# Performance work log

Hardware: AMD Instinct MI355X
Metric: run time of the kernel (lower is better)

The kernel has to match this reference:

```python
import jax, jax.numpy as jnp
import numpy as np

# Dims per init_kwargs
B, C_IN, H, W = 64, 512, 28, 28
GROWTH, BN_SIZE = 32, 4
C_MID = BN_SIZE * GROWTH  # 128
EPS = 1e-5
NUM_BITS = 8          # activation & weight quantization bits
NUM_CHUNKS = 16       # RangeBN chunking (eladhoffer quantize.py default)


def quantize(x, num_bits):
    """Uniform min/max quantize-dequantize (UniformQuantize forward)."""
    mn = x.min()
    mx = x.max()
    qmax = 2.0 ** num_bits - 1.0
    scale = jnp.maximum((mx - mn) / qmax, 1e-8)
    q = jnp.round((jnp.clip(x, mn, mx) - mn) / scale)
    return q * scale + mn


def conv2d(x, w, pad):
    return jax.lax.conv_general_dilated(
        x, w, window_strides=(1, 1), padding=[(pad, pad), (pad, pad)],
        dimension_numbers=('NCHW', 'OIHW', 'NCHW'))


def batchnorm2d(x, w, b):
    # training-mode BN: batch statistics over (N,H,W), biased variance
    mean = x.mean(axis=(0, 2, 3), keepdims=True)
    var = x.var(axis=(0, 2, 3), keepdims=True)
    xhat = (x - mean) * jax.lax.rsqrt(var + EPS)
    return xhat * w.reshape(1, -1, 1, 1) + b.reshape(1, -1, 1, 1)


def range_bn(x, w, b):
    # Range-based BN (training-mode): per-channel mean, scale from chunked min/max range
    Bx, Cx, Hx, Wx = x.shape
    y = x.transpose(1, 0, 2, 3).reshape(Cx, NUM_CHUNKS, -1)  # [C, chunks, n]
    mean_max = y.max(-1).mean(-1)   # [C]
    mean_min = y.min(-1).mean(-1)   # [C]
    mean = y.reshape(Cx, -1).mean(-1)  # [C]
    n = y.shape[-1]
    scale_fix = (0.5 * 0.35) * (1.0 + (np.pi * np.log(4.0)) ** 0.5) / ((2.0 * np.log(float(n))) ** 0.5)
    scale = 1.0 / ((mean_max - mean_min) * scale_fix + EPS)
    out = (x - mean.reshape(1, Cx, 1, 1)) * scale.reshape(1, Cx, 1, 1)
    qw = quantize(w, NUM_BITS)
    qb = quantize(b, NUM_BITS)
    return out * qw.reshape(1, Cx, 1, 1) + qb.reshape(1, Cx, 1, 1)


def setup_inputs() -> dict:
    key = jax.random.key(0)
    ks = jax.random.split(key, 7)
    x = jax.random.normal(ks[0], (B, C_IN, H, W), dtype=jnp.float32)
    bn1_w = jax.random.uniform(ks[1], (C_IN,), dtype=jnp.float32, minval=0.5, maxval=1.5)
    bn1_b = jax.random.normal(ks[2], (C_IN,), dtype=jnp.float32) * 0.1
    conv1_w = jax.random.normal(ks[3], (C_MID, C_IN, 1, 1), dtype=jnp.float32) * (2.0 / C_IN) ** 0.5
    rbn_w = jax.random.uniform(ks[4], (C_MID,), dtype=jnp.float32, minval=0.5, maxval=1.5)
    rbn_b = jax.random.normal(ks[5], (C_MID,), dtype=jnp.float32) * 0.1
    conv2_w = jax.random.normal(ks[6], (GROWTH, C_MID, 3, 3), dtype=jnp.float32) * (2.0 / (9 * C_MID)) ** 0.5
    return {"x": x, "bn1_w": bn1_w, "bn1_b": bn1_b, "conv1_w": conv1_w,
            "rbn_w": rbn_w, "rbn_b": rbn_b, "conv2_w": conv2_w}


def reference(x, bn1_w, bn1_b, conv1_w, rbn_w, rbn_b, conv2_w):
    # norm1 -> relu1 -> QConv2d(1x1) -> RangeBN -> relu2 -> QConv2d(3x3) -> concat
    h = jax.nn.relu(batchnorm2d(x, bn1_w, bn1_b))
    h = conv2d(quantize(h, NUM_BITS), quantize(conv1_w, NUM_BITS), pad=0)
    h = jax.nn.relu(range_bn(h, rbn_w, rbn_b))
    h = conv2d(quantize(h, NUM_BITS), quantize(conv2_w, NUM_BITS), pad=1)
    # drop_rate = 0 -> dropout is identity
    return jnp.concatenate([x, h], axis=1)
```

## Files before the change

kernel.cpp:

```cpp
#include <hip/hip_runtime.h>
#include <math.h>

static constexpr int BB    = 64;
static constexpr int C_IN  = 512;
static constexpr int C_MID = 128;
static constexpr int C_OUT = 32;
static constexpr int C_TOT = 544;
static constexpr int HW    = 784;

static constexpr size_t H2_OFF    = 0;
static constexpr size_t QW1_OFF   = 6422528;
static constexpr size_t QW2_OFF   = QW1_OFF + 65536;
static constexpr size_t PSTAT_OFF = QW2_OFF + 49152;
static constexpr size_t BNA_OFF   = PSTAT_OFF + 16384;
static constexpr size_t BNB_OFF   = BNA_OFF + 512;
static constexpr size_t A2_OFF    = BNB_OFF + 512;
static constexpr size_t B2_OFF    = A2_OFF + 128;
static constexpr size_t QRW_OFF   = B2_OFF + 128;
static constexpr size_t QRB_OFF   = QRW_OFF + 128;
static constexpr size_t SCAL_OFF  = QRB_OFF + 128;
static constexpr size_t PART_OFF  = SCAL_OFF + 16;
static constexpr size_t RP_OFF    = PART_OFF + 128;
static constexpr size_t PART2_OFF = RP_OFF + 172032;

#define DEVFN __device__ __forceinline__

typedef __bf16 bf16x8 __attribute__((ext_vector_type(8)));
typedef float  f32x4  __attribute__((ext_vector_type(4)));

DEVFN float qact(float v, float mn, float mx, float inv, float sc) {
    v = fminf(fmaxf(v, mn), mx);
    return fmaf(rintf((v - mn) * inv), sc, mn);
}

DEVFN unsigned f2bf(float f) {
    unsigned u = __float_as_uint(f);
    return (u + 0x7fffu + ((u >> 16) & 1u)) >> 16;
}

DEVFN float bf2f(unsigned short h) { return __uint_as_float((unsigned)h << 16); }

__global__ __launch_bounds__(256) void k_stats(const float* __restrict__ x,
                                               const float* __restrict__ conv1_w,
                                               const float* __restrict__ conv2_w,
                                               float* __restrict__ ws) {
    const int bid = blockIdx.x, tid = threadIdx.x;
    __shared__ float r0[256], r1[256], r2[256], r3[256];

    if (bid < 4096) {
        const int xcd = bid & 7, slot = bid >> 3;
        const int c = xcd * 64 + (slot & 63), bg = slot >> 6;
        float s = 0.f, s2 = 0.f, mn = INFINITY, mx = -INFINITY;
        for (int i = tid; i < 1568; i += 256) {
            const int b = bg * 8 + i / 196, j = i % 196;
            const float4 v = ((const float4*)(x + ((size_t)b * C_IN + c) * HW))[j];
            s  += (v.x + v.y) + (v.z + v.w);
            s2 += v.x * v.x + v.y * v.y + v.z * v.z + v.w * v.w;
            mn = fminf(mn, fminf(fminf(v.x, v.y), fminf(v.z, v.w)));
            mx = fmaxf(mx, fmaxf(fmaxf(v.x, v.y), fmaxf(v.z, v.w)));
        }
        r0[tid] = s; r1[tid] = s2; r2[tid] = mn; r3[tid] = mx;
        __syncthreads();
        for (int off = 128; off > 0; off >>= 1) {
            if (tid < off) {
                r0[tid] += r0[tid + off];
                r1[tid] += r1[tid + off];
                r2[tid] = fminf(r2[tid], r2[tid + off]);
                r3[tid] = fmaxf(r3[tid], r3[tid + off]);
            }
            __syncthreads();
        }
        if (tid == 0) {
            float* p = ws + PSTAT_OFF + ((size_t)c * 8 + bg) * 4;
            p[0] = r0[0]; p[1] = r1[0]; p[2] = r2[0]; p[3] = r3[0];
        }
    } else {
        const int wb = bid - 4096;
        float mn = INFINITY, mx = -INFINITY;
        if (wb < 32) {
            const float4* src = (const float4*)conv1_w + (size_t)wb * 512;
            for (int i = tid; i < 512; i += 256) {
                const float4 v = src[i];
                mn = fminf(mn, fminf(fminf(v.x, v.y), fminf(v.z, v.w)));
                mx = fmaxf(mx, fmaxf(fmaxf(v.x, v.y), fmaxf(v.z, v.w)));
            }
        } else {
            const float4* src = (const float4*)conv2_w + (size_t)(wb - 32) * 1152;
            for (int i = tid; i < 1152; i += 256) {
                const float4 v = src[i];
                mn = fminf(mn, fminf(fminf(v.x, v.y), fminf(v.z, v.w)));
                mx = fmaxf(mx, fmaxf(fmaxf(v.x, v.y), fmaxf(v.z, v.w)));
            }
        }
        r2[tid] = mn; r3[tid] = mx;
        __syncthreads();
        for (int off = 128; off > 0; off >>= 1) {
            if (tid < off) { r2[tid] = fminf(r2[tid], r2[tid + off]); r3[tid] = fmaxf(r3[tid], r3[tid + off]); }
            __syncthreads();
        }
        if (tid == 0) {
            float* p = (wb < 32) ? ws + PART_OFF + (size_t)wb * 2
                                 : ws + PART_OFF + 64 + (size_t)(wb - 32) * 2;
            p[0] = r2[0]; p[1] = r3[0];
        }
    }
}

__global__ __launch_bounds__(256) void k_prep(const float* __restrict__ conv1_w,
                                              const float* __restrict__ conv2_w,
                                              const float* __restrict__ bn1_w,
                                              const float* __restrict__ bn1_b,
                                              const float* __restrict__ rbn_w,
                                              const float* __restrict__ rbn_b,
                                              float* __restrict__ ws) {
    const int b = blockIdx.x, tid = threadIdx.x;
    __shared__ float ra[256], rb[256];
    __shared__ float s_mn, s_sc;

    if (b < 32) {
        ra[tid] = tid < 32 ? ws[PART_OFF + tid * 2] : INFINITY;
        rb[tid] = tid < 32 ? ws[PART_OFF + tid * 2 + 1] : -INFINITY;
        __syncthreads();
        for (int off = 128; off > 0; off >>= 1) {
            if (tid < off) { ra[tid] = fminf(ra[tid], ra[tid + off]); rb[tid] = fmaxf(rb[tid], rb[tid + off]); }
            __syncthreads();
        }
        if (tid == 0) { s_mn = ra[0]; s_sc = fmaxf((rb[0] - ra[0]) / 255.f, 1e-8f); }
        __syncthreads();
        const float mnw = s_mn, scw = s_sc;
        unsigned short* qw = (unsigned short*)(ws + QW1_OFF);
        const int base = b * 2048;
#pragma unroll
        for (int t = 0; t < 8; ++t) {
            const int i = base + t * 256 + tid;
            const int co = i >> 9, k = i & 511;
            const float v = conv1_w[i];
            const float qv = fmaf(rintf((v - mnw) / scw), scw, mnw);
            const int ks = k >> 6, kc = (k >> 3) & 7, klo = k & 7;
            qw[(((size_t)ks * 128 + co) << 6) + (((kc ^ (co & 7)) << 3) | klo)] = (unsigned short)f2bf(qv);
        }
    } else if (b < 40) {
        ra[tid] = tid < 8 ? ws[PART_OFF + 64 + tid * 2] : INFINITY;
        rb[tid] = tid < 8 ? ws[PART_OFF + 64 + tid * 2 + 1] : -INFINITY;
        __syncthreads();
        for (int off = 128; off > 0; off >>= 1) {
            if (tid < off) { ra[tid] = fminf(ra[tid], ra[tid + off]); rb[tid] = fmaxf(rb[tid], rb[tid + off]); }
            __syncthreads();
        }
        if (tid == 0) { s_mn = ra[0]; s_sc = fmaxf((rb[0] - ra[0]) / 255.f, 1e-8f); }
        __syncthreads();
        const float mnw = s_mn, scw = s_sc;
        unsigned short* qw2 = (unsigned short*)(ws + QW2_OFF);
        const int base = (b - 32) * 4608;
        for (int i2 = tid; i2 < 4608; i2 += 256) {
            const int i = base + i2;
            const int co = i / 1152, r = i % 1152, ci = r / 9, tap = r % 9;
            const float v = conv2_w[i];
            const float qv = fmaf(rintf((v - mnw) / scw), scw, mnw);
            qw2[(size_t)co * 1152 + tap * 128 + ci] = (unsigned short)f2bf(qv);
        }
    } else if (b == 40) {
        float lmn = INFINITY, lmx = -INFINITY;
        for (int c = tid; c < 512; c += 256) {
            const float* p = ws + PSTAT_OFF + (size_t)c * 32;
            float s = 0.f, s2 = 0.f, cmn = INFINITY, cmx = -INFINITY;
            for (int g = 0; g < 8; ++g) {
                s += p[g * 4 + 0]; s2 += p[g * 4 + 1];
                cmn = fminf(cmn, p[g * 4 + 2]); cmx = fmaxf(cmx, p[g * 4 + 3]);
            }
            const float n = 50176.f;
            const float mean = s / n;
            const float var  = s2 / n - mean * mean;
            const float rstd = rsqrtf(var + 1e-5f);
            const float A  = rstd * bn1_w[c];
            const float Bc = bn1_b[c] - mean * A;
            ws[BNA_OFF + c] = A; ws[BNB_OFF + c] = Bc;
            const float v1 = A * cmn + Bc, v2 = A * cmx + Bc;
            lmn = fminf(lmn, fmaxf(0.f, fminf(v1, v2)));
            lmx = fmaxf(lmx, fmaxf(0.f, fmaxf(v1, v2)));
        }
        ra[tid] = lmn; rb[tid] = lmx;
        __syncthreads();
        for (int off = 128; off > 0; off >>= 1) {
            if (tid < off) { ra[tid] = fminf(ra[tid], ra[tid + off]); rb[tid] = fmaxf(rb[tid], rb[tid + off]); }
            __syncthreads();
        }
        if (tid == 0) {
            const float mn1 = ra[0], mx1 = rb[0];
            const float sc = fmaxf((mx1 - mn1) / 255.f, 1e-8f);
            ws[SCAL_OFF + 0] = mn1; ws[SCAL_OFF + 1] = sc; ws[SCAL_OFF + 2] = 1.f / sc; ws[SCAL_OFF + 6] = mx1;
        }
    } else {
        for (int which = 0; which < 2; ++which) {
            const float* src = which ? rbn_b : rbn_w;
            const size_t dst = which ? QRB_OFF : QRW_OFF;
            float v = 0.f;
            ra[tid] = INFINITY; rb[tid] = -INFINITY;
            if (tid < 128) { v = src[tid]; ra[tid] = v; rb[tid] = v; }
            __syncthreads();
            for (int off = 128; off > 0; off >>= 1) {
                if (tid < off) { ra[tid] = fminf(ra[tid], ra[tid + off]); rb[tid] = fmaxf(rb[tid], rb[tid + off]); }
                __syncthreads();
            }
            if (tid == 0) { s_mn = ra[0]; s_sc = fmaxf((rb[0] - ra[0]) / 255.f, 1e-8f); }
            __syncthreads();
            if (tid < 128) ws[dst + tid] = fmaf(rintf((v - s_mn) / s_sc), s_sc, s_mn);
            __syncthreads();
        }
    }
}

__global__ __launch_bounds__(256, 2) void k_conv1(const float* __restrict__ x,
                                                  float* __restrict__ out,
                                                  float* __restrict__ ws) {
    __shared__ __align__(16) unsigned short wt[128 * 64];
    __shared__ __align__(16) unsigned short ht[112 * 64];
    const int tid = threadIdx.x;
    const int pt = blockIdx.x, b = blockIdx.y;
    const int p0 = pt * 112;
    const float mn1 = ws[SCAL_OFF + 0], sc1 = ws[SCAL_OFF + 1];
    const float inv1 = ws[SCAL_OFF + 2];
    const unsigned short* qw1 = (const unsigned short*)(ws + QW1_OFF);
    const float* xb = x + (size_t)b * C_IN * HW;
    float* outb = out + (size_t)b * C_TOT * HW;

    const int o = tid & 7, q = tid >> 3;
    const int wv = tid >> 6, g = (tid >> 4) & 3, r4 = tid & 15;

    f32x4 acc[2][7];
#pragma unroll
    for (int i = 0; i < 2; ++i)
#pragma unroll
        for (int j = 0; j < 7; ++j) acc[i][j] = f32x4{0.f, 0.f, 0.f, 0.f};

    f32x4 xreg[8];
    if (tid < 224) {
#pragma unroll
        for (int j = 0; j < 8; ++j)
            xreg[j] = *(const f32x4*)(xb + (size_t)(o * 8 + j) * HW + p0 + q * 4);
    }

    for (int ks = 0; ks < 8; ++ks) {
        const float4* wsrc = (const float4*)(qw1 + (size_t)ks * 8192);
        float4* wdst = (float4*)wt;
#pragma unroll
        for (int i = 0; i < 4; ++i) wdst[tid + i * 256] = wsrc[tid + i * 256];

        if (tid < 224) {
            const int ci0 = ks * 64 + o * 8;
            float vv[8][4];
#pragma unroll
            for (int j = 0; j < 8; ++j) {
                const f32x4 v = xreg[j];
                __builtin_nontemporal_store(v, (f32x4*)(outb + (size_t)(ci0 + j) * HW + p0 + q * 4));
                const float A = ws[BNA_OFF + ci0 + j], Bc = ws[BNB_OFF + ci0 + j];
                vv[j][0] = fmaf(rintf((fmaxf(fmaf(v.x, A, Bc), 0.f) - mn1) * inv1), sc1, mn1);
                vv[j][1] = fmaf(rintf((fmaxf(fmaf(v.y, A, Bc), 0.f) - mn1) * inv1), sc1, mn1);
                vv[j][2] = fmaf(rintf((fmaxf(fmaf(v.z, A, Bc), 0.f) - mn1) * inv1), sc1, mn1);
                vv[j][3] = fmaf(rintf((fmaxf(fmaf(v.w, A, Bc), 0.f) - mn1) * inv1), sc1, mn1);
            }
            if (ks < 7) {
                const int ci0n = (ks + 1) * 64 + o * 8;
#pragma unroll
                for (int j = 0; j < 8; ++j)
                    xreg[j] = *(const f32x4*)(xb + (size_t)(ci0n + j) * HW + p0 + q * 4);
            }
#pragma unroll
            for (int r = 0; r < 4; ++r) {
                const int p = q * 4 + r;
                uint4 pk;
                pk.x = f2bf(vv[0][r]) | (f2bf(vv[1][r]) << 16);
                pk.y = f2bf(vv[2][r]) | (f2bf(vv[3][r]) << 16);
                pk.z = f2bf(vv[4][r]) | (f2bf(vv[5][r]) << 16);
                pk.w = f2bf(vv[6][r]) | (f2bf(vv[7][r]) << 16);
                *(uint4*)&ht[p * 64 + ((o ^ (p & 7)) << 3)] = pk;
            }
        }
        __syncthreads();

#pragma unroll
        for (int ksub = 0; ksub < 2; ++ksub) {
            const int kk = ksub * 4 + g;
            bf16x8 af[2], bfr[7];
#pragma unroll
            for (int ct = 0; ct < 2; ++ct) {
                const int co = wv * 32 + ct * 16 + r4;
                af[ct] = *(const bf16x8*)&wt[co * 64 + ((kk ^ (co & 7)) << 3)];
            }
#pragma unroll
            for (int pf = 0; pf < 7; ++pf) {
                const int p = pf * 16 + r4;
                bfr[pf] = *(const bf16x8*)&ht[p * 64 + ((kk ^ (p & 7)) << 3)];
            }
#pragma unroll
            for (int ct = 0; ct < 2; ++ct)
#pragma unroll
                for (int pf = 0; pf < 7; ++pf)
                    acc[ct][pf] = __builtin_amdgcn_mfma_f32_16x16x32_bf16(af[ct], bfr[pf], acc[ct][pf], 0, 0, 0);
        }
        __syncthreads();
    }

    unsigned short* hb = (unsigned short*)(ws + H2_OFF) + (size_t)b * C_MID * HW;
#pragma unroll
    for (int ct = 0; ct < 2; ++ct) {
        const int co0 = wv * 32 + ct * 16 + g * 4;
#pragma unroll
        for (int pf = 0; pf < 7; ++pf) {
            const int p = p0 + pf * 16 + r4;
#pragma unroll
            for (int r = 0; r < 4; ++r)
                hb[(size_t)(co0 + r) * HW + p] = (unsigned short)f2bf(acc[ct][pf][r]);
        }
    }

#pragma unroll
    for (int ct = 0; ct < 2; ++ct)
#pragma unroll
        for (int r = 0; r < 4; ++r) {
            float s = 0.f, mn = INFINITY, mx = -INFINITY;
#pragma unroll
            for (int pf = 0; pf < 7; ++pf) {
                const float v = acc[ct][pf][r];
                s += v; mn = fminf(mn, v); mx = fmaxf(mx, v);
            }
#pragma unroll
            for (int m = 1; m < 16; m <<= 1) {
                s  += __shfl_xor(s, m, 64);
                mn  = fminf(mn, __shfl_xor(mn, m, 64));
                mx  = fmaxf(mx, __shfl_xor(mx, m, 64));
            }
            if (r4 == 0) {
                const int co = wv * 32 + ct * 16 + g * 4 + r;
                float* dst = ws + RP_OFF + (((size_t)co * 64 + b) * 7 + pt) * 3;
                dst[0] = s; dst[1] = mn; dst[2] = mx;
            }
        }
}

__global__ __launch_bounds__(64) void k_rbn_combine(float* __restrict__ ws) {
    const int c = blockIdx.x, t = threadIdx.x;
    const int ch = t >> 2, sub = t & 3;
    const int b = ch * 4 + sub;
    const float* rp = ws + RP_OFF + ((size_t)c * 64 + b) * 21;
    float s = 0.f, mn = INFINITY, mx = -INFINITY;
#pragma unroll
    for (int pt = 0; pt < 7; ++pt) {
        s += rp[pt * 3 + 0];
        mn = fminf(mn, rp[pt * 3 + 1]);
        mx = fmaxf(mx, rp[pt * 3 + 2]);
    }
#pragma unroll
    for (int m = 1; m < 4; m <<= 1) {
        s  += __shfl_xor(s, m, 64);
        mn  = fminf(mn, __shfl_xor(mn, m, 64));
        mx  = fmaxf(mx, __shfl_xor(mx, m, 64));
    }
    float smx = mx, smn = mn, stot = s, gmn = mn, gmx = mx;
#pragma unroll
    for (int m = 4; m < 64; m <<= 1) {
        smx  += __shfl_xor(smx, m, 64);
        smn  += __shfl_xor(smn, m, 64);
        stot += __shfl_xor(stot, m, 64);
        gmn   = fminf(gmn, __shfl_xor(gmn, m, 64));
        gmx   = fmaxf(gmx, __shfl_xor(gmx, m, 64));
    }
    if (t == 0) {
        const float mm = smx * (1.f / 16.f), mnm = smn * (1.f / 16.f);
        const float mean = stot / 50176.f;
        const double PI_D = 3.14159265358979323846;
        const double sfd = 0.175 * (1.0 + sqrt(PI_D * log(4.0))) / sqrt(2.0 * log(3136.0));
        const float scale = 1.f / ((mm - mnm) * (float)sfd + 1e-5f);
        const float A  = scale * ws[QRW_OFF + c];
        const float Bc = ws[QRB_OFF + c] - mean * A;
        ws[A2_OFF + c] = A; ws[B2_OFF + c] = Bc;
        const float v1 = A * gmn + Bc, v2 = A * gmx + Bc;
        ws[PART2_OFF + c * 2 + 0] = fmaxf(0.f, fminf(v1, v2));
        ws[PART2_OFF + c * 2 + 1] = fmaxf(0.f, fmaxf(v1, v2));
    }
}

__global__ __launch_bounds__(256, 2) void k_conv2(float* __restrict__ out, const float* __restrict__ ws) {
    __shared__ __align__(16) unsigned short lact[7 * 30 * 128];
    __shared__ float sra[128], srb[128];
    __shared__ float s_mn3, s_mx3, s_sc3, s_inv3;
    const int tid = threadIdx.x;
    const int pt = blockIdx.x, b = blockIdx.y;
    const int y0 = pt * 4;

    if (tid < 128) { sra[tid] = ws[PART2_OFF + tid * 2]; srb[tid] = ws[PART2_OFF + tid * 2 + 1]; }
    __syncthreads();
    for (int off = 64; off > 0; off >>= 1) {
        if (tid < off) { sra[tid] = fminf(sra[tid], sra[tid + off]); srb[tid] = fmaxf(srb[tid], srb[tid + off]); }
        __syncthreads();
    }
    if (tid == 0) {
        const float mn3 = sra[0], mx3 = srb[0];
        const float sc = fmaxf((mx3 - mn3) / 255.f, 1e-8f);
        s_mn3 = mn3; s_mx3 = mx3; s_sc3 = sc; s_inv3 = 1.f / sc;
    }
    {
        const uint4 z = {0u, 0u, 0u, 0u};
        uint4* lp = (uint4*)lact;
        for (int i = tid; i < 3360; i += 256) lp[i] = z;
    }
    __syncthreads();
    const float mn3 = s_mn3, mx3 = s_mx3, sc3 = s_sc3, inv3 = s_inv3;

    const unsigned short* h2b = (const unsigned short*)(ws + H2_OFF) + (size_t)b * C_MID * HW;
    for (int task = tid; task < 672; task += 256) {
        const int oct = task / 42, rem = task % 42, r = rem / 7, xq = rem % 7;
        const int gy = y0 - 1 + r;
        if (gy < 0 || gy > 27) continue;
        float vv[8][4];
#pragma unroll
        for (int j = 0; j < 8; ++j) {
            const int ci = oct * 8 + j;
            const ushort4 v = *(const ushort4*)(h2b + (size_t)ci * HW + gy * 28 + xq * 4);
            const float A = ws[A2_OFF + ci], Bc = ws[B2_OFF + ci];
            vv[j][0] = qact(fmaxf(0.f, fmaf(bf2f(v.x), A, Bc)), mn3, mx3, inv3, sc3);
            vv[j][1] = qact(fmaxf(0.f, fmaf(bf2f(v.y), A, Bc)), mn3, mx3, inv3, sc3);
            vv[j][2] = qact(fmaxf(0.f, fmaf(bf2f(v.z), A, Bc)), mn3, mx3, inv3, sc3);
            vv[j][3] = qact(fmaxf(0.f, fmaf(bf2f(v.w), A, Bc)), mn3, mx3, inv3, sc3);
        }
#pragma unroll
        for (int xi = 0; xi < 4; ++xi) {
            const int col = xq * 4 + xi + 1;
            const int phys = (oct + col) & 15;
            uint4 pk;
            pk.x = f2bf(vv[0][xi]) | (f2bf(vv[1][xi]) << 16);
            pk.y = f2bf(vv[2][xi]) | (f2bf(vv[3][xi]) << 16);
            pk.z = f2bf(vv[4][xi]) | (f2bf(vv[5][xi]) << 16);
            pk.w = f2bf(vv[6][xi]) | (f2bf(vv[7][xi]) << 16);
            *(uint4*)&lact[((r * 30 + col) * 16 + phys) * 8] = pk;
        }
    }
    __syncthreads();

    const int wv = tid >> 6, lane = tid & 63, r4 = lane & 15, g = lane >> 4;
    int py[2], px[2];
#pragma unroll
    for (int i = 0; i < 2; ++i) {
        const int p = (wv * 2 + i) * 16 + r4;
        py[i] = p / 28; px[i] = p % 28;
    }
    f32x4 acc[2][2];
#pragma unroll
    for (int ct = 0; ct < 2; ++ct)
#pragma unroll
        for (int i = 0; i < 2; ++i) acc[ct][i] = f32x4{0.f, 0.f, 0.f, 0.f};

    const unsigned short* qw2 = (const unsigned short*)(ws + QW2_OFF);
    for (int tap = 0; tap < 9; ++tap) {
        const int dy = tap / 3, dx = tap % 3;
        bf16x8 afr[2][4];
#pragma unroll
        for (int ct = 0; ct < 2; ++ct)
#pragma unroll
            for (int c4 = 0; c4 < 4; ++c4) {
                const int co = ct * 16 + r4;
                afr[ct][c4] = *(const bf16x8*)&qw2[(size_t)co * 1152 + tap * 128 + c4 * 32 + g * 8];
            }
#pragma unroll
        for (int c4 = 0; c4 < 4; ++c4) {
            bf16x8 bfr[2];
#pragma unroll
            for (int i = 0; i < 2; ++i) {
                const int row = py[i] + dy, col = px[i] + dx;
                const int phys = (c4 * 4 + g + col) & 15;
                bfr[i] = *(const bf16x8*)&lact[((row * 30 + col) * 16 + phys) * 8];
            }
#pragma unroll
            for (int ct = 0; ct < 2; ++ct)
#pragma unroll
                for (int i = 0; i < 2; ++i)
                    acc[ct][i] = __builtin_amdgcn_mfma_f32_16x16x32_bf16(afr[ct][c4], bfr[i], acc[ct][i], 0, 0, 0);
        }
    }

#pragma unroll
    for (int ct = 0; ct < 2; ++ct)
#pragma unroll
        for (int i = 0; i < 2; ++i) {
            const int pf = wv * 2 + i;
            if (pf < 7) {
                const int p = pf * 16 + r4;
#pragma unroll
                for (int r = 0; r < 4; ++r) {
                    const int co = ct * 16 + g * 4 + r;
                    out[((size_t)b * C_TOT + 512 + co) * HW + y0 * 28 + p] = acc[ct][i][r];
                }
            }
        }
}

extern "C" void kernel_launch(void* const* d_in, const int* in_sizes, int n_in,
                              void* d_out, int out_size, void* d_ws, size_t ws_size,
                              hipStream_t stream) {
    const float* x       = (const float*)d_in[0];
    const float* bn1_w   = (const float*)d_in[1];
    const float* bn1_b   = (const float*)d_in[2];
    const float* conv1_w = (const float*)d_in[3];
    const float* rbn_w   = (const float*)d_in[4];
    const float* rbn_b   = (const float*)d_in[5];
    const float* conv2_w = (const float*)d_in[6];
    float* out = (float*)d_out;
    float* ws  = (float*)d_ws;

    k_stats<<<4136, 256, 0, stream>>>(x, conv1_w, conv2_w, ws);
    k_prep<<<42, 256, 0, stream>>>(conv1_w, conv2_w, bn1_w, bn1_b, rbn_w, rbn_b, ws);
    k_conv1<<<dim3(7, 64), 256, 0, stream>>>(x, out, ws);
    k_rbn_combine<<<128, 64, 0, stream>>>(ws);
    k_conv2<<<dim3(7, 64), 256, 0, stream>>>(out, ws);
}
```

Before: 103.2 us.

## Store intermediate activations channel-last via LDS transpose for coalesced conv2 staging

The conv1 epilogue now transposes its bf16 accumulator tile through shared memory so the intermediate tensor is written in pixel-major (NHWC) layout with 16-byte coalesced stores, replacing scattered 2-byte channel-major writes. The conv2 staging loop reads 8 contiguous channels per pixel with one 16-byte load and takes per-channel affine coefficients from shared memory instead of repeated global loads. This targets uncoalesced global traffic in both kernels, at the cost of an extra LDS round trip and barrier in conv1.

```diff
diff --git a/kernel.cpp b/kernel.cpp
--- a/kernel.cpp
+++ b/kernel.cpp
@@ -213,8 +213,9 @@
 __global__ __launch_bounds__(256, 2) void k_conv1(const float* __restrict__ x,
                                                   float* __restrict__ out,
                                                   float* __restrict__ ws) {
-    __shared__ __align__(16) unsigned short wt[128 * 64];
-    __shared__ __align__(16) unsigned short ht[112 * 64];
+    __shared__ __align__(16) unsigned short smem[8192 + 7168];
+    unsigned short* wt = smem;
+    unsigned short* ht = smem + 8192;
     const int tid = threadIdx.x;
     const int pt = blockIdx.x, b = blockIdx.y;
     const int p0 = pt * 112;
@@ -301,17 +302,28 @@
         __syncthreads();
     }
 
-    unsigned short* hb = (unsigned short*)(ws + H2_OFF) + (size_t)b * C_MID * HW;
 #pragma unroll
     for (int ct = 0; ct < 2; ++ct) {
-        const int co0 = wv * 32 + ct * 16 + g * 4;
+        const int co = wv * 32 + ct * 16 + g * 4;
+        const int grp = co >> 3, lo = co & 7;
 #pragma unroll
         for (int pf = 0; pf < 7; ++pf) {
-            const int p = p0 + pf * 16 + r4;
-#pragma unroll
-            for (int r = 0; r < 4; ++r)
-                hb[(size_t)(co0 + r) * HW + p] = (unsigned short)f2bf(acc[ct][pf][r]);
-        }
+            const int p = pf * 16 + r4;
+            uint2 pv;
+            pv.x = f2bf(acc[ct][pf][0]) | (f2bf(acc[ct][pf][1]) << 16);
+            pv.y = f2bf(acc[ct][pf][2]) | (f2bf(acc[ct][pf][3]) << 16);
+            *(uint2*)&smem[p * 128 + ((grp ^ (p & 15)) << 3) + lo] = pv;
+        }
+    }
+    __syncthreads();
+
+    unsigned short* hb = (unsigned short*)(ws + H2_OFF) + (size_t)b * HW * C_MID;
+#pragma unroll
+    for (int k2 = 0; k2 < 7; ++k2) {
+        const int idx = k2 * 256 + tid;
+        const int p = idx >> 4, grp = idx & 15;
+        const uint4 v = *(const uint4*)&smem[p * 128 + ((grp ^ (p & 15)) << 3)];
+        *(uint4*)&hb[(size_t)(p0 + p) * C_MID + grp * 8] = v;
     }
 
 #pragma unroll
@@ -383,12 +395,16 @@
 __global__ __launch_bounds__(256, 2) void k_conv2(float* __restrict__ out, const float* __restrict__ ws) {
     __shared__ __align__(16) unsigned short lact[7 * 30 * 128];
     __shared__ float sra[128], srb[128];
+    __shared__ float sA[128], sB[128];
     __shared__ float s_mn3, s_mx3, s_sc3, s_inv3;
     const int tid = threadIdx.x;
     const int pt = blockIdx.x, b = blockIdx.y;
     const int y0 = pt * 4;
 
-    if (tid < 128) { sra[tid] = ws[PART2_OFF + tid * 2]; srb[tid] = ws[PART2_OFF + tid * 2 + 1]; }
+    if (tid < 128) {
+        sra[tid] = ws[PART2_OFF + tid * 2]; srb[tid] = ws[PART2_OFF + tid * 2 + 1];
+        sA[tid] = ws[A2_OFF + tid]; sB[tid] = ws[B2_OFF + tid];
+    }
     __syncthreads();
     for (int off = 64; off > 0; off >>= 1) {
         if (tid < off) { sra[tid] = fminf(sra[tid], sra[tid + off]); srb[tid] = fmaxf(srb[tid], srb[tid + off]); }
@@ -407,33 +423,26 @@
     __syncthreads();
     const float mn3 = s_mn3, mx3 = s_mx3, sc3 = s_sc3, inv3 = s_inv3;
 
-    const unsigned short* h2b = (const unsigned short*)(ws + H2_OFF) + (size_t)b * C_MID * HW;
-    for (int task = tid; task < 672; task += 256) {
-        const int oct = task / 42, rem = task % 42, r = rem / 7, xq = rem % 7;
+    const unsigned short* h2b = (const unsigned short*)(ws + H2_OFF) + (size_t)b * HW * C_MID;
+    for (int i = tid; i < 2688; i += 256) {
+        const int pos = i >> 4, grp = i & 15;
+        const int r = pos / 28, gx = pos % 28;
         const int gy = y0 - 1 + r;
         if (gy < 0 || gy > 27) continue;
-        float vv[8][4];
-#pragma unroll
-        for (int j = 0; j < 8; ++j) {
-            const int ci = oct * 8 + j;
-            const ushort4 v = *(const ushort4*)(h2b + (size_t)ci * HW + gy * 28 + xq * 4);
-            const float A = ws[A2_OFF + ci], Bc = ws[B2_OFF + ci];
-            vv[j][0] = qact(fmaxf(0.f, fmaf(bf2f(v.x), A, Bc)), mn3, mx3, inv3, sc3);
-            vv[j][1] = qact(fmaxf(0.f, fmaf(bf2f(v.y), A, Bc)), mn3, mx3, inv3, sc3);
-            vv[j][2] = qact(fmaxf(0.f, fmaf(bf2f(v.z), A, Bc)), mn3, mx3, inv3, sc3);
-            vv[j][3] = qact(fmaxf(0.f, fmaf(bf2f(v.w), A, Bc)), mn3, mx3, inv3, sc3);
-        }
-#pragma unroll
-        for (int xi = 0; xi < 4; ++xi) {
-            const int col = xq * 4 + xi + 1;
-            const int phys = (oct + col) & 15;
-            uint4 pk;
-            pk.x = f2bf(vv[0][xi]) | (f2bf(vv[1][xi]) << 16);
-            pk.y = f2bf(vv[2][xi]) | (f2bf(vv[3][xi]) << 16);
-            pk.z = f2bf(vv[4][xi]) | (f2bf(vv[5][xi]) << 16);
-            pk.w = f2bf(vv[6][xi]) | (f2bf(vv[7][xi]) << 16);
-            *(uint4*)&lact[((r * 30 + col) * 16 + phys) * 8] = pk;
-        }
+        const uint4 hv = *(const uint4*)(h2b + (size_t)(gy * 28 + gx) * C_MID + grp * 8);
+        const unsigned hw[4] = {hv.x, hv.y, hv.z, hv.w};
+        unsigned pk[4];
+#pragma unroll
+        for (int w2 = 0; w2 < 4; ++w2) {
+            const int ci = grp * 8 + w2 * 2;
+            const float a0 = qact(fmaxf(0.f, fmaf(bf2f((unsigned short)(hw[w2] & 0xffffu)), sA[ci], sB[ci])), mn3, mx3, inv3, sc3);
+            const float a1 = qact(fmaxf(0.f, fmaf(bf2f((unsigned short)(hw[w2] >> 16)), sA[ci + 1], sB[ci + 1])), mn3, mx3, inv3, sc3);
+            pk[w2] = f2bf(a0) | (f2bf(a1) << 16);
+        }
+        const int col = gx + 1;
+        const int phys = (grp + col) & 15;
+        uint4 ov; ov.x = pk[0]; ov.y = pk[1]; ov.z = pk[2]; ov.w = pk[3];
+        *(uint4*)&lact[((r * 30 + col) * 16 + phys) * 8] = ov;
     }
     __syncthreads();
 
```

Measured after the change: 104.3 us. Within noise of the previous version (+1.1%).
